# Performance work log

Hardware: AMD Instinct MI355X
Metric: run time of the kernel (lower is better)

The kernel has to match this reference:

```python
import jax, jax.numpy as jnp
import numpy as np

N_NODES = 100000
N_EDGES = 1600000
N_GRAPHS = 256
DIMS = [128, 128, 128, 128]  # gcn_layers_dim -> 3 GCNConv layers


def setup_inputs() -> dict:
    key = jax.random.key(0)
    ks = jax.random.split(key, 12)
    inp = {
        "x": jax.random.normal(ks[0], (N_NODES, DIMS[0]), jnp.float32),
        "edge_index": jax.random.randint(ks[1], (2, N_EDGES), 0, N_NODES),
        "edge_weight": jax.random.uniform(ks[2], (N_EDGES,), jnp.float32),
        "batch": jnp.sort(jax.random.randint(ks[3], (N_NODES,), 0, N_GRAPHS)),
    }
    for i in range(3):
        fan_in = DIMS[i]
        scale = 1.0 / np.sqrt(fan_in)
        inp[f"W{i+1}"] = jax.random.uniform(ks[4 + 2 * i], (DIMS[i], DIMS[i + 1]),
                                             jnp.float32, -scale, scale)
        inp[f"b{i+1}"] = jax.random.uniform(ks[5 + 2 * i], (DIMS[i + 1],),
                                             jnp.float32, -scale, scale)
    return inp


def reference(x, edge_index, edge_weight, batch, W1, b1, W2, b2, W3, b3):
    n = x.shape[0]
    # PyG GCNConv: add self-loops with weight 1, symmetric normalization.
    loop = jnp.arange(n)
    row = jnp.concatenate([edge_index[0], loop])  # source nodes
    col = jnp.concatenate([edge_index[1], loop])  # target nodes (aggregation index)
    w = jnp.concatenate([edge_weight, jnp.ones((n,), x.dtype)])
    deg = jax.ops.segment_sum(w, col, num_segments=n)
    dinv = jnp.where(deg > 0, jax.lax.rsqrt(deg), jnp.zeros_like(deg))
    norm = dinv[row] * w * dinv[col]  # [E+N]

    # global_mean_pool setup
    counts = jax.ops.segment_sum(jnp.ones((n,), x.dtype), batch,
                                 num_segments=N_GRAPHS)
    counts = jnp.maximum(counts, 1.0)[:, None]

    def gcn_conv(h, W, b):
        hl = h @ W                      # linear projection first (PyG order)
        msg = hl[row] * norm[:, None]   # gather + edge scaling
        out = jax.ops.segment_sum(msg, col, num_segments=n)  # scatter-add
        return out + b

    embeddings = []
    h = x
    for W, b in ((W1, b1), (W2, b2), (W3, b3)):
        h = gcn_conv(h, W, b)
        h = jax.nn.relu(h)              # relu_layers_index = [0,1,2]
        emb = jax.ops.segment_sum(h, batch, num_segments=N_GRAPHS) / counts
        embeddings.append(emb)          # gep = global_mean_pool
    return tuple(embeddings)
```

## Files before the change

### kernel.cpp

```cpp
#include <hip/hip_runtime.h>


typedef short short8 __attribute__((ext_vector_type(8)));
typedef float f32x4  __attribute__((ext_vector_type(4)));

__device__ inline unsigned pack_bf16x2(float a, float b) {
    unsigned ua = __float_as_uint(a);
    ua = (ua + 0x7FFFu + ((ua >> 16) & 1u)) >> 16;
    unsigned ub = __float_as_uint(b);
    ub = (ub + 0x7FFFu + ((ub >> 16) & 1u)) >> 16;
    return ua | (ub << 16);
}
__device__ inline ushort bf16_1(float a) {
    unsigned ua = __float_as_uint(a);
    return (ushort)((ua + 0x7FFFu + ((ua >> 16) & 1u)) >> 16);
}
__device__ inline float bf_lo(unsigned u) { return __uint_as_float(u << 16); }
__device__ inline float bf_hi(unsigned u) { return __uint_as_float(u & 0xFFFF0000u); }


template <bool F32IN>
__device__ __forceinline__ void gemm_tile(const void* __restrict__ Hin,
                                          const ushort* __restrict__ WbT,
                                          unsigned* __restrict__ O, int M,
                                          int bid, unsigned* sOut) {
    int lane = threadIdx.x & 63;
    int wv = threadIdx.x >> 6;
    int quad = lane >> 4;
    int mrow = lane & 15;
    int m0 = bid * 128 + wv * 32;
    int r0 = m0 + mrow;
    int r1 = r0 + 16;
    int r0c = r0 < M ? r0 : M - 1;
    int r1c = r1 < M ? r1 : M - 1;

    short8 a0[4], a1[4];
    if (F32IN) {
        const float* Hf = (const float*)Hin;
#pragma unroll
        for (int s = 0; s < 4; s++) {
            const float4* p0 = (const float4*)(Hf + (size_t)r0c * 128 + s * 32 + quad * 8);
            const float4* p1 = (const float4*)(Hf + (size_t)r1c * 128 + s * 32 + quad * 8);
            float4 f0 = p0[0], f1 = p0[1];
            float4 g0 = p1[0], g1 = p1[1];
            union { short8 s8; unsigned u[4]; } t0, t1;
            t0.u[0] = pack_bf16x2(f0.x, f0.y); t0.u[1] = pack_bf16x2(f0.z, f0.w);
            t0.u[2] = pack_bf16x2(f1.x, f1.y); t0.u[3] = pack_bf16x2(f1.z, f1.w);
            t1.u[0] = pack_bf16x2(g0.x, g0.y); t1.u[1] = pack_bf16x2(g0.z, g0.w);
            t1.u[2] = pack_bf16x2(g1.x, g1.y); t1.u[3] = pack_bf16x2(g1.z, g1.w);
            a0[s] = t0.s8; a1[s] = t1.s8;
        }
    } else {
        const unsigned* Hb = (const unsigned*)Hin;
#pragma unroll
        for (int s = 0; s < 4; s++) {
            a0[s] = *(const short8*)(Hb + (size_t)r0c * 64 + s * 16 + quad * 4);
            a1[s] = *(const short8*)(Hb + (size_t)r1c * 64 + s * 16 + quad * 4);
        }
    }
    f32x4 acc0[8], acc1[8];
#pragma unroll
    for (int t = 0; t < 8; t++) {
        acc0[t] = (f32x4){0.f, 0.f, 0.f, 0.f};
        acc1[t] = (f32x4){0.f, 0.f, 0.f, 0.f};
    }
#pragma unroll
    for (int s = 0; s < 4; s++) {
#pragma unroll
        for (int t = 0; t < 8; t++) {
            short8 b = *(const short8*)(WbT + (t * 16 + mrow) * 128 + s * 32 + quad * 8);
            acc0[t] = __builtin_amdgcn_mfma_f32_16x16x32_bf16(a0[s], b, acc0[t], 0, 0, 0);
            acc1[t] = __builtin_amdgcn_mfma_f32_16x16x32_bf16(a1[s], b, acc1[t], 0, 0, 0);
        }
    }
    ushort* so = (ushort*)(sOut + wv * 32 * 64);
#pragma unroll
    for (int t = 0; t < 8; t++) {
#pragma unroll
        for (int r = 0; r < 4; r++) {
            int lr = quad * 4 + r;
            int c = t * 16 + mrow;
            so[lr * 128 + c] = bf16_1(acc0[t][r]);
            so[(lr + 16) * 128 + c] = bf16_1(acc1[t][r]);
        }
    }
    __syncthreads();
    const unsigned* si = sOut + wv * 32 * 64;
#pragma unroll 8
    for (int r = 0; r < 32; r++) {
        int row = m0 + r;
        if (row < M) O[(size_t)row * 64 + lane] = si[r * 64 + lane];
    }
}

__device__ __forceinline__ void pool_tile(const unsigned* __restrict__ HB,
                                          const int* __restrict__ gb,
                                          float* __restrict__ outp, int g,
                                          float* part) {
    int lane = threadIdx.x & 63, w = threadIdx.x >> 6;
    int s = gb[g], e = gb[g + 1];
    float ax = 0.f, ay = 0.f;
    for (int i = s + w; i < e; i += 4) {
        unsigned u = HB[(size_t)i * 64 + lane];
        ax += bf_lo(u); ay += bf_hi(u);
    }
    part[w * 128 + lane * 2] = ax;
    part[w * 128 + lane * 2 + 1] = ay;
    __syncthreads();
    if (threadIdx.x < 128) {
        float sum = part[threadIdx.x] + part[128 + threadIdx.x]
                  + part[256 + threadIdx.x] + part[384 + threadIdx.x];
        float c = (float)(e - s);
        outp[g * 128 + threadIdx.x] = sum / fmaxf(c, 1.0f);
    }
}


__global__ void k_prep(unsigned long long* __restrict__ lines, int N,
                       int* __restrict__ bsum,
                       const int* __restrict__ batch, int* __restrict__ gb, int G,
                       const float* __restrict__ W0, const float* __restrict__ W1,
                       const float* __restrict__ W2, ushort* __restrict__ WbT) {
    int id = blockIdx.x * blockDim.x + threadIdx.x;
    if (id < N) lines[(size_t)id * 8] = 0ULL;
    if (id < 128) bsum[id] = 0;
    if (id <= G) {
        int lo = 0, hi = N;
        while (lo < hi) { int mid = (lo + hi) >> 1; if (batch[mid] < id) lo = mid + 1; else hi = mid; }
        gb[id] = lo;
    }
    if (id < 3 * 16384) {
        int l = id >> 14;
        const float* W = (l == 0) ? W0 : ((l == 1) ? W1 : W2);
        int id2 = id & 16383;
        int n = id2 & 127, k = id2 >> 7;
        WbT[l * 16384 + n * 128 + k] = bf16_1(W[k * 128 + n]);
    }
}

__global__ __launch_bounds__(256) void k_phase1(const int* __restrict__ ei,
                                                const float* __restrict__ ew,
                                                unsigned long long* __restrict__ lines,
                                                int E,
                                                const float* __restrict__ x,
                                                const ushort* __restrict__ WbT,
                                                unsigned* __restrict__ O, int M,
                                                int nbGemm) {
    __shared__ unsigned sBuf[8192];
    if (blockIdx.x < nbGemm) {
        gemm_tile<true>(x, WbT, O, M, blockIdx.x, sBuf);
        return;
    }
    int base = (blockIdx.x - nbGemm) * 1024 + threadIdx.x;
#pragma unroll
    for (int q = 0; q < 4; q++) {
        int e = base + q * 256;
        if (e < E) {
            int c = ei[E + e];
            float w = ew[e];
            unsigned long long pkt =
                (1ULL << 40) | (unsigned long long)(unsigned)(w * 4194304.0f + 0.5f);
            atomicAdd(&lines[(size_t)c * 8], pkt);
        }
    }
}

__global__ __launch_bounds__(1024) void k_scan1(unsigned long long* __restrict__ lines,
                                                int* __restrict__ pre,
                                                int* __restrict__ bsum,
                                                float* __restrict__ dinv, int n) {
    __shared__ int wsum[16];
    int t = threadIdx.x, lane = t & 63, w = t >> 6;
    int i = blockIdx.x * 1024 + t;
    int v = 0; float dg = 1.0f;
    if (i < n) {
        unsigned long long u = lines[(size_t)i * 8];
        v = (int)(u >> 40);
        dg = 1.0f + (float)(u & 0xFFFFFFFFFFULL) * (1.0f / 4194304.0f);
    }
    int x = v;
#pragma unroll
    for (int off = 1; off < 64; off <<= 1) {
        int y = __shfl_up(x, off, 64);
        if (lane >= off) x += y;
    }
    if (lane == 63) wsum[w] = x;
    __syncthreads();
    int woff = 0, tot = 0;
#pragma unroll
    for (int q = 0; q < 16; q++) { int s = wsum[q]; if (q < w) woff += s; tot += s; }
    if (i < n) {
        int ex = woff + x - v;
        pre[i] = ex;
        ((int*)lines)[(size_t)i * 16] = ex;
        dinv[i] = rsqrtf(dg);
    }
    if (t == 0) bsum[blockIdx.x] = tot;
}

__global__ __launch_bounds__(256) void k_scatter(const int* __restrict__ ei,
                                                 const float* __restrict__ ew,
                                                 const int* __restrict__ pre,
                                                 const int* __restrict__ bsumRaw,
                                                 int* __restrict__ ptrv,
                                                 const float* __restrict__ dinv,
                                                 int* __restrict__ cur,
                                                 int2* __restrict__ csr, int E, int N) {
    __shared__ int sRaw[256];
    __shared__ int sPre[256];
    __shared__ int sWt[4];
    int t = threadIdx.x;
    sRaw[t] = (t < 128) ? bsumRaw[t] : 0;
    __syncthreads();
    int lane = t & 63, w2 = t >> 6;
    int v = sRaw[t];
    int x = v;
#pragma unroll
    for (int off = 1; off < 64; off <<= 1) {
        int y = __shfl_up(x, off, 64);
        if (lane >= off) x += y;
    }
    if (lane == 63) sWt[w2] = x;
    __syncthreads();
    int base = 0;
#pragma unroll
    for (int q = 0; q < 4; q++) { if (q < w2) base += sWt[q]; }
    sPre[t] = base + x - v;
    __syncthreads();
    int e = blockIdx.x * 256 + t;
    if (e < N) ptrv[e] = pre[e] + sPre[e >> 10];
    if (e == 0) ptrv[N] = sWt[0] + sWt[1];
    if (e >= E) return;
    int r = ei[e];
    int c = ei[E + e];
    float y = dinv[r] * ew[e] * dinv[c];
    int slot = sPre[c >> 10] + atomicAdd(&cur[(size_t)c * 16], 1);
    int2 mv; mv.x = r; mv.y = __float_as_int(y);
    csr[slot] = mv;
}

__global__ __launch_bounds__(256) void k_agg(const unsigned* __restrict__ HL,
                                             const int* __restrict__ ptr,
                                             const int2* __restrict__ csr,
                                             const float* __restrict__ dinv,
                                             const float* __restrict__ bias,
                                             unsigned* __restrict__ Hout, int M) {
    __shared__ int2 sM[4 * 64];
    int node = (int)((blockIdx.x * blockDim.x + threadIdx.x) >> 6);
    if (node >= M) return;
    int lane = threadIdx.x & 63;
    int half = lane >> 5;
    int q = lane & 31;
    int2* mbase = &sM[(threadIdx.x >> 6) * 64];
    int e0 = ptr[node], e1 = ptr[node + 1];
    int deg = e1 - e0;
    int nbv = deg < 64 ? deg : 64;
    if (lane < nbv) mbase[lane] = csr[e0 + lane];
    const uint2* HL2 = (const uint2*)HL;
    float di = dinv[node];
    float sn = (half == 0) ? di * di : 0.f;
    uint2 us = HL2[(size_t)node * 32 + q];
    float a0 = sn * bf_lo(us.x), a1 = sn * bf_hi(us.x);
    float a2 = sn * bf_lo(us.y), a3 = sn * bf_hi(us.y);
    int j = half;
    for (; j + 8 <= nbv; j += 8) {
        int2 m[4]; uint2 u[4];
#pragma unroll
        for (int t = 0; t < 4; t++) m[t] = mbase[j + 2 * t];
#pragma unroll
        for (int t = 0; t < 4; t++) u[t] = HL2[(size_t)m[t].x * 32 + q];
#pragma unroll
        for (int t = 0; t < 4; t++) {
            float nv = __int_as_float(m[t].y);
            a0 += nv * bf_lo(u[t].x); a1 += nv * bf_hi(u[t].x);
            a2 += nv * bf_lo(u[t].y); a3 += nv * bf_hi(u[t].y);
        }
    }
    for (; j < nbv; j += 2) {
        int2 m = mbase[j];
        uint2 u = HL2[(size_t)m.x * 32 + q];
        float nv = __int_as_float(m.y);
        a0 += nv * bf_lo(u.x); a1 += nv * bf_hi(u.x);
        a2 += nv * bf_lo(u.y); a3 += nv * bf_hi(u.y);
    }
    for (int e = e0 + 64 + half; e < e1; e += 2) {
        int2 m = csr[e];
        uint2 u = HL2[(size_t)m.x * 32 + q];
        float nv = __int_as_float(m.y);
        a0 += nv * bf_lo(u.x); a1 += nv * bf_hi(u.x);
        a2 += nv * bf_lo(u.y); a3 += nv * bf_hi(u.y);
    }
    a0 += __shfl_xor(a0, 32, 64);
    a1 += __shfl_xor(a1, 32, 64);
    a2 += __shfl_xor(a2, 32, 64);
    a3 += __shfl_xor(a3, 32, 64);
    float4 bv = ((const float4*)bias)[q];
    float r0 = fmaxf(a0 + bv.x, 0.f);
    float r1 = fmaxf(a1 + bv.y, 0.f);
    float r2 = fmaxf(a2 + bv.z, 0.f);
    float r3 = fmaxf(a3 + bv.w, 0.f);
    if (half == 0) {
        uint2 pv;
        pv.x = pack_bf16x2(r0, r1);
        pv.y = pack_bf16x2(r2, r3);
        ((uint2*)(Hout + (size_t)node * 64))[q] = pv;
    }
}

__global__ __launch_bounds__(256) void k_gemm_pool(const unsigned* __restrict__ Hb,
                                                   const ushort* __restrict__ WbT,
                                                   unsigned* __restrict__ O, int M,
                                                   const int* __restrict__ gb,
                                                   float* __restrict__ outp,
                                                   int nbGemm) {
    __shared__ unsigned sBuf[8192];
    if (blockIdx.x < nbGemm) {
        gemm_tile<false>(Hb, WbT, O, M, blockIdx.x, sBuf);
        return;
    }
    pool_tile(Hb, gb, outp, blockIdx.x - nbGemm, (float*)sBuf);
}

extern "C" void kernel_launch(void* const* d_in, const int* in_sizes, int n_in,
                              void* d_out, int out_size, void* d_ws, size_t ws_size,
                              hipStream_t stream) {
    const float* x     = (const float*)d_in[0];
    const int*   ei    = (const int*)d_in[1];
    const float* ew    = (const float*)d_in[2];
    const int*   batch = (const int*)d_in[3];
    const float* Wt[3] = {(const float*)d_in[4], (const float*)d_in[6], (const float*)d_in[8]};
    const float* bt[3] = {(const float*)d_in[5], (const float*)d_in[7], (const float*)d_in[9]};
    float* out = (float*)d_out;

    const int D = 128;
    const int N = in_sizes[0] / D;
    const int E = in_sizes[2];
    const int G = out_size / (3 * D);

    char* p = (char*)d_ws;
    auto alloc = [&](size_t bytes) {
        void* r = (void*)p;
        p += (bytes + 255) & ~(size_t)255;
        return r;
    };
    int*      ptr    = (int*)alloc((size_t)(N + 1) * 4);
    int*      pre    = (int*)alloc((size_t)N * 4);
    int*      bsum   = (int*)alloc((size_t)128 * 4);
    int*      gb     = (int*)alloc((size_t)(G + 1) * 4);
    float*    dinv   = (float*)alloc((size_t)N * 4);
    ushort*   WbT    = (ushort*)alloc((size_t)3 * 16384 * 2);
    int2*     csr    = (int2*)alloc((size_t)E * 8);
    unsigned* bufHL  = (unsigned*)alloc((size_t)N * 64 * 4);
    unsigned* bufH   = (unsigned*)alloc((size_t)N * 64 * 4);
    unsigned long long* lines = (unsigned long long*)bufH;

    int nb = (N + 1023) / 1024;
    int nbGemm = (N + 127) / 128;
    int nbAtomic = (E + 1023) / 1024;
    int prepWork = N > 3 * 16384 ? N : 3 * 16384;

    k_prep<<<(prepWork + 255) / 256, 256, 0, stream>>>(lines, N, bsum, batch, gb, G,
                                                       Wt[0], Wt[1], Wt[2], WbT);
    k_phase1<<<nbGemm + nbAtomic, 256, 0, stream>>>(ei, ew, lines, E,
                                                    x, WbT, bufHL, N, nbGemm);
    k_scan1<<<nb, 1024, 0, stream>>>(lines, pre, bsum, dinv, N);
    k_scatter<<<(E + 255) / 256, 256, 0, stream>>>(ei, ew, pre, bsum, ptr, dinv,
                                                   (int*)lines, csr, E, N);

    k_agg<<<(N + 3) / 4, 256, 0, stream>>>(bufHL, ptr, csr, dinv, bt[0], bufH, N);
    k_gemm_pool<<<nbGemm + G, 256, 0, stream>>>(bufH, WbT + 16384, bufHL, N,
                                                gb, out + 0 * (size_t)G * D, nbGemm);
    k_agg<<<(N + 3) / 4, 256, 0, stream>>>(bufHL, ptr, csr, dinv, bt[1], bufH, N);
    k_gemm_pool<<<nbGemm + G, 256, 0, stream>>>(bufH, WbT + 2 * 16384, bufHL, N,
                                                gb, out + 1 * (size_t)G * D, nbGemm);
    k_agg<<<(N + 3) / 4, 256, 0, stream>>>(bufHL, ptr, csr, dinv, bt[2], bufH, N);
    k_gemm_pool<<<G, 256, 0, stream>>>(bufH, WbT, nullptr, 0,
                                       gb, out + 2 * (size_t)G * D, 0);
}
```

Before: 586.3 us.

## Build CSR via two-level bucketed counting sort instead of global atomics

Replaces per-node global atomic degree counting and atomic CSR scatter with a bucket (128-node) histogram in shared memory, a scan over bucket×block counts, a bucketed record scatter, then a per-bucket local sort that computes degrees, dinv and row pointers. The source-side normalization is applied in a separate pass over the CSR. This is meant to remove contended global atomics and random scattered writes, at the cost of extra kernels and extra passes over edge records. It also drops the fixed-point degree encoding in favour of float shared-memory accumulation.

```diff
diff --git a/kernel.cpp b/kernel.cpp
--- a/kernel.cpp
+++ b/kernel.cpp
@@ -116,14 +116,11 @@
 }
 
 
-__global__ void k_prep(unsigned long long* __restrict__ lines, int N,
-                       int* __restrict__ bsum,
-                       const int* __restrict__ batch, int* __restrict__ gb, int G,
+__global__ void k_prep(const int* __restrict__ batch, int* __restrict__ gb,
+                       int G, int N,
                        const float* __restrict__ W0, const float* __restrict__ W1,
                        const float* __restrict__ W2, ushort* __restrict__ WbT) {
     int id = blockIdx.x * blockDim.x + threadIdx.x;
-    if (id < N) lines[(size_t)id * 8] = 0ULL;
-    if (id < 128) bsum[id] = 0;
     if (id <= G) {
         int lo = 0, hi = N;
         while (lo < hi) { int mid = (lo + hi) >> 1; if (batch[mid] < id) lo = mid + 1; else hi = mid; }
@@ -139,104 +136,178 @@
 }
 
 __global__ __launch_bounds__(256) void k_phase1(const int* __restrict__ ei,
-                                                const float* __restrict__ ew,
-                                                unsigned long long* __restrict__ lines,
-                                                int E,
+                                                int* __restrict__ hist, int E,
                                                 const float* __restrict__ x,
                                                 const ushort* __restrict__ WbT,
                                                 unsigned* __restrict__ O, int M,
-                                                int nbGemm) {
+                                                int nbGemm, int nbCount) {
     __shared__ unsigned sBuf[8192];
     if (blockIdx.x < nbGemm) {
         gemm_tile<true>(x, WbT, O, M, blockIdx.x, sBuf);
         return;
     }
-    int base = (blockIdx.x - nbGemm) * 1024 + threadIdx.x;
+    int blk = blockIdx.x - nbGemm;
+    unsigned* hcnt = sBuf;
+    int t = threadIdx.x;
+    for (int i = t; i < nbGemm; i += 256) hcnt[i] = 0;
+    __syncthreads();
+    int base = blk * 8192;
+    for (int i = t; i < 8192; i += 256) {
+        int e = base + i;
+        if (e < E) atomicAdd(&hcnt[(unsigned)ei[E + e] >> 7], 1u);
+    }
+    __syncthreads();
+    for (int b = t; b < nbGemm; b += 256)
+        hist[b * nbCount + blk] = (int)hcnt[b];
+}
+
+__global__ __launch_bounds__(1024) void k_scan1(const int* __restrict__ cnt,
+                                                int* __restrict__ pre,
+                                                int* __restrict__ bsum, int n) {
+    __shared__ int wsum[16];
+    int t = threadIdx.x, lane = t & 63, w = t >> 6;
+    int i = blockIdx.x * 1024 + t;
+    int v = (i < n) ? cnt[i] : 0;
+    int x = v;
+#pragma unroll
+    for (int off = 1; off < 64; off <<= 1) {
+        int y = __shfl_up(x, off, 64);
+        if (lane >= off) x += y;
+    }
+    if (lane == 63) wsum[w] = x;
+    __syncthreads();
+    int woff = 0, tot = 0;
+#pragma unroll
+    for (int q = 0; q < 16; q++) { int s = wsum[q]; if (q < w) woff += s; tot += s; }
+    if (i < n) pre[i] = woff + x - v;
+    if (t == 0) bsum[blockIdx.x] = tot;
+}
+
+__global__ __launch_bounds__(256) void k_scat(const int* __restrict__ ei,
+                                              const float* __restrict__ ew,
+                                              const int* __restrict__ pre,
+                                              const int* __restrict__ bsumRaw,
+                                              int* __restrict__ bucketStart,
+                                              int2* __restrict__ recs,
+                                              int E, int nbkt, int nbCount,
+                                              int nbScan) {
+    __shared__ int sRaw[256];
+    __shared__ int sPre[256];
+    __shared__ int sWt[4];
+    __shared__ int sBase[784];
+    __shared__ unsigned rk[784];
+    int t = threadIdx.x;
+    sRaw[t] = (t < nbScan) ? bsumRaw[t] : 0;
+    for (int b = t; b < nbkt; b += 256) rk[b] = 0;
+    __syncthreads();
+    int lane = t & 63, w2 = t >> 6;
+    int v = sRaw[t];
+    int x = v;
+#pragma unroll
+    for (int off = 1; off < 64; off <<= 1) {
+        int y = __shfl_up(x, off, 64);
+        if (lane >= off) x += y;
+    }
+    if (lane == 63) sWt[w2] = x;
+    __syncthreads();
+    int base = 0;
+#pragma unroll
+    for (int q = 0; q < 4; q++) { if (q < w2) base += sWt[q]; }
+    sPre[t] = base + x - v;
+    __syncthreads();
+    int blk = blockIdx.x;
+    for (int b = t; b < nbkt; b += 256) {
+        int f = b * nbCount + blk;
+        sBase[b] = pre[f] + sPre[f >> 10];
+    }
+    if (blk == 0) {
+        for (int b = t; b <= nbkt; b += 256) {
+            if (b == nbkt) bucketStart[b] = E;
+            else { int f = b * nbCount; bucketStart[b] = pre[f] + sPre[f >> 10]; }
+        }
+    }
+    __syncthreads();
+    int e0 = blk * 8192;
+    for (int i = t; i < 8192; i += 256) {
+        int e = e0 + i;
+        if (e < E) {
+            int r = ei[e];
+            int c = ei[E + e];
+            float w = ew[e];
+            int b = (unsigned)c >> 7;
+            unsigned rank = atomicAdd(&rk[b], 1u);
+            int2 rec; rec.x = r | ((c & 127) << 17); rec.y = __float_as_int(w);
+            recs[sBase[b] + (int)rank] = rec;
+        }
+    }
+}
+
+__global__ __launch_bounds__(256) void k_fin(const int2* __restrict__ recs,
+                                             const int* __restrict__ bucketStart,
+                                             int2* __restrict__ csr,
+                                             int* __restrict__ ptrv,
+                                             float* __restrict__ dinv,
+                                             int N, int nbkt) {
+    __shared__ unsigned scnt[128];
+    __shared__ float swdeg[128];
+    __shared__ float sdinv[128];
+    __shared__ unsigned sTot0;
+    int t = threadIdx.x;
+    int b = blockIdx.x;
+    int e0 = bucketStart[b], e1 = bucketStart[b + 1];
+    if (t < 128) { scnt[t] = 0u; swdeg[t] = 0.f; }
+    __syncthreads();
+    for (int i = e0 + t; i < e1; i += 256) {
+        int2 rec = recs[i];
+        int cl = (rec.x >> 17) & 127;
+        atomicAdd(&scnt[cl], 1u);
+        atomicAdd(&swdeg[cl], __int_as_float(rec.y));
+    }
+    __syncthreads();
+    unsigned myc = (t < 128) ? scnt[t] : 0u;
+    int lane = t & 63, wv = t >> 6;
+    unsigned inc = myc;
+#pragma unroll
+    for (int off = 1; off < 64; off <<= 1) {
+        unsigned y = __shfl_up(inc, off, 64);
+        if (lane >= off) inc += y;
+    }
+    if (t == 63) sTot0 = inc;
+    __syncthreads();
+    unsigned excl = inc - myc + ((wv == 1) ? sTot0 : 0u);
+    if (t < 128) {
+        scnt[t] = excl;
+        float dv = rsqrtf(1.0f + swdeg[t]);
+        sdinv[t] = dv;
+        int node = b * 128 + t;
+        if (node < N) { ptrv[node] = e0 + (int)excl; dinv[node] = dv; }
+    }
+    if (b == nbkt - 1 && t == 0) ptrv[N] = e1;
+    __syncthreads();
+    for (int i = e0 + t; i < e1; i += 256) {
+        int2 rec = recs[i];
+        int cl = (rec.x >> 17) & 127;
+        int r = rec.x & 131071;
+        unsigned rank = atomicAdd(&scnt[cl], 1u);
+        float y = __int_as_float(rec.y) * sdinv[cl];
+        int2 mv; mv.x = r; mv.y = __float_as_int(y);
+        csr[e0 + (int)rank] = mv;
+    }
+}
+
+__global__ __launch_bounds__(256) void k_norm2(int2* __restrict__ csr,
+                                               const float* __restrict__ dinv,
+                                               int E) {
+    int base = blockIdx.x * 1024 + threadIdx.x;
 #pragma unroll
     for (int q = 0; q < 4; q++) {
         int e = base + q * 256;
         if (e < E) {
-            int c = ei[E + e];
-            float w = ew[e];
-            unsigned long long pkt =
-                (1ULL << 40) | (unsigned long long)(unsigned)(w * 4194304.0f + 0.5f);
-            atomicAdd(&lines[(size_t)c * 8], pkt);
-        }
-    }
-}
-
-__global__ __launch_bounds__(1024) void k_scan1(unsigned long long* __restrict__ lines,
-                                                int* __restrict__ pre,
-                                                int* __restrict__ bsum,
-                                                float* __restrict__ dinv, int n) {
-    __shared__ int wsum[16];
-    int t = threadIdx.x, lane = t & 63, w = t >> 6;
-    int i = blockIdx.x * 1024 + t;
-    int v = 0; float dg = 1.0f;
-    if (i < n) {
-        unsigned long long u = lines[(size_t)i * 8];
-        v = (int)(u >> 40);
-        dg = 1.0f + (float)(u & 0xFFFFFFFFFFULL) * (1.0f / 4194304.0f);
-    }
-    int x = v;
-#pragma unroll
-    for (int off = 1; off < 64; off <<= 1) {
-        int y = __shfl_up(x, off, 64);
-        if (lane >= off) x += y;
-    }
-    if (lane == 63) wsum[w] = x;
-    __syncthreads();
-    int woff = 0, tot = 0;
-#pragma unroll
-    for (int q = 0; q < 16; q++) { int s = wsum[q]; if (q < w) woff += s; tot += s; }
-    if (i < n) {
-        int ex = woff + x - v;
-        pre[i] = ex;
-        ((int*)lines)[(size_t)i * 16] = ex;
-        dinv[i] = rsqrtf(dg);
-    }
-    if (t == 0) bsum[blockIdx.x] = tot;
-}
-
-__global__ __launch_bounds__(256) void k_scatter(const int* __restrict__ ei,
-                                                 const float* __restrict__ ew,
-                                                 const int* __restrict__ pre,
-                                                 const int* __restrict__ bsumRaw,
-                                                 int* __restrict__ ptrv,
-                                                 const float* __restrict__ dinv,
-                                                 int* __restrict__ cur,
-                                                 int2* __restrict__ csr, int E, int N) {
-    __shared__ int sRaw[256];
-    __shared__ int sPre[256];
-    __shared__ int sWt[4];
-    int t = threadIdx.x;
-    sRaw[t] = (t < 128) ? bsumRaw[t] : 0;
-    __syncthreads();
-    int lane = t & 63, w2 = t >> 6;
-    int v = sRaw[t];
-    int x = v;
-#pragma unroll
-    for (int off = 1; off < 64; off <<= 1) {
-        int y = __shfl_up(x, off, 64);
-        if (lane >= off) x += y;
-    }
-    if (lane == 63) sWt[w2] = x;
-    __syncthreads();
-    int base = 0;
-#pragma unroll
-    for (int q = 0; q < 4; q++) { if (q < w2) base += sWt[q]; }
-    sPre[t] = base + x - v;
-    __syncthreads();
-    int e = blockIdx.x * 256 + t;
-    if (e < N) ptrv[e] = pre[e] + sPre[e >> 10];
-    if (e == 0) ptrv[N] = sWt[0] + sWt[1];
-    if (e >= E) return;
-    int r = ei[e];
-    int c = ei[E + e];
-    float y = dinv[r] * ew[e] * dinv[c];
-    int slot = sPre[c >> 10] + atomicAdd(&cur[(size_t)c * 16], 1);
-    int2 mv; mv.x = r; mv.y = __float_as_int(y);
-    csr[slot] = mv;
+            int2 m = csr[e];
+            m.y = __float_as_int(__int_as_float(m.y) * dinv[m.x]);
+            csr[e] = m;
+        }
+    }
 }
 
 __global__ __launch_bounds__(256) void k_agg(const unsigned* __restrict__ HL,
@@ -343,29 +414,36 @@
         p += (bytes + 255) & ~(size_t)255;
         return r;
     };
+    int nbkt    = (N + 127) / 128;
+    int nbCount = (E + 8191) / 8192;
+    int F       = nbkt * nbCount;
+    int nbScan  = (F + 1023) / 1024;
+
     int*      ptr    = (int*)alloc((size_t)(N + 1) * 4);
-    int*      pre    = (int*)alloc((size_t)N * 4);
-    int*      bsum   = (int*)alloc((size_t)128 * 4);
+    int*      bsum   = (int*)alloc((size_t)256 * 4);
     int*      gb     = (int*)alloc((size_t)(G + 1) * 4);
+    int*      bstart = (int*)alloc((size_t)(nbkt + 1) * 4);
     float*    dinv   = (float*)alloc((size_t)N * 4);
     ushort*   WbT    = (ushort*)alloc((size_t)3 * 16384 * 2);
     int2*     csr    = (int2*)alloc((size_t)E * 8);
     unsigned* bufHL  = (unsigned*)alloc((size_t)N * 64 * 4);
     unsigned* bufH   = (unsigned*)alloc((size_t)N * 64 * 4);
-    unsigned long long* lines = (unsigned long long*)bufH;
-
-    int nb = (N + 1023) / 1024;
+    int*  hist = (int*)csr;
+    int*  pre  = hist + F;
+    int2* recs = (int2*)bufH;
+
     int nbGemm = (N + 127) / 128;
-    int nbAtomic = (E + 1023) / 1024;
-    int prepWork = N > 3 * 16384 ? N : 3 * 16384;
-
-    k_prep<<<(prepWork + 255) / 256, 256, 0, stream>>>(lines, N, bsum, batch, gb, G,
+    int prepWork = 3 * 16384;
+
+    k_prep<<<(prepWork + 255) / 256, 256, 0, stream>>>(batch, gb, G, N,
                                                        Wt[0], Wt[1], Wt[2], WbT);
-    k_phase1<<<nbGemm + nbAtomic, 256, 0, stream>>>(ei, ew, lines, E,
-                                                    x, WbT, bufHL, N, nbGemm);
-    k_scan1<<<nb, 1024, 0, stream>>>(lines, pre, bsum, dinv, N);
-    k_scatter<<<(E + 255) / 256, 256, 0, stream>>>(ei, ew, pre, bsum, ptr, dinv,
-                                                   (int*)lines, csr, E, N);
+    k_phase1<<<nbGemm + nbCount, 256, 0, stream>>>(ei, hist, E, x, WbT,
+                                                   bufHL, N, nbGemm, nbCount);
+    k_scan1<<<nbScan, 1024, 0, stream>>>(hist, pre, bsum, F);
+    k_scat<<<nbCount, 256, 0, stream>>>(ei, ew, pre, bsum, bstart, recs,
+                                        E, nbkt, nbCount, nbScan);
+    k_fin<<<nbkt, 256, 0, stream>>>(recs, bstart, csr, ptr, dinv, N, nbkt);
+    k_norm2<<<(E + 1023) / 1024, 256, 0, stream>>>(csr, dinv, E);
 
     k_agg<<<(N + 3) / 4, 256, 0, stream>>>(bufHL, ptr, csr, dinv, bt[0], bufH, N);
     k_gemm_pool<<<nbGemm + G, 256, 0, stream>>>(bufH, WbT + 16384, bufHL, N,
```

Result: faster. 524.5 us (-10.5%).
